# Optimization experiments

Measured on AMD Instinct MI355X. Metric: run time of the kernel, lower is better.

Reference implementation:

```python
import jax, jax.numpy as jnp
import numpy as np

N = 10000
IN_DIM = 512
OUT_DIM = 128
E = 262144


def setup_inputs() -> dict:
    key = jax.random.key(0)
    ks = jax.random.split(key, 7)
    x = jax.random.normal(ks[0], (N, IN_DIM), dtype=jnp.float32)
    adj = jax.random.uniform(ks[1], (N, N), dtype=jnp.float32) * (1.0 / N)
    # xavier-ish scaled params
    weight = jax.random.normal(ks[2], (IN_DIM, OUT_DIM), dtype=jnp.float32) * (1.0 / np.sqrt(IN_DIM))
    weight_two = jax.random.normal(ks[3], (2 * OUT_DIM, OUT_DIM), dtype=jnp.float32) * (1.0 / np.sqrt(2 * OUT_DIM))
    weight_three = jax.random.normal(ks[4], (2 * OUT_DIM, 1), dtype=jnp.float32) * (1.0 / np.sqrt(2 * OUT_DIM))
    train_edges = jax.random.randint(ks[5], (E, 2), 0, N, dtype=jnp.int32)
    train_false_edges = jax.random.randint(ks[6], (E, 2), 0, N, dtype=jnp.int32)
    return {
        "x": x,
        "adj": adj,
        "weight": weight,
        "weight_two": weight_two,
        "weight_three": weight_three,
        "train_edges": train_edges,
        "train_false_edges": train_false_edges,
    }


def reference(x, adj, weight, weight_two, weight_three, train_edges, train_false_edges):
    # encode: z = adj @ (x @ W)   -> [N, OUT_DIM]
    z = adj @ (x @ weight)
    # decode: vectorized per-edge gather of both endpoints
    edges = jnp.concatenate([train_edges, train_false_edges], axis=0)  # [2E, 2]
    zi = z[edges[:, 0]]  # [2E, OUT_DIM]
    zj = z[edges[:, 1]]  # [2E, OUT_DIM]
    z_pair = jnp.concatenate([zi, zj], axis=1)          # [2E, 2*OUT_DIM]
    z_mult = zi * zj                                     # [2E, OUT_DIM]
    z_pair = jax.nn.relu(z_pair) @ weight_two            # [2E, OUT_DIM]
    logits = jnp.concatenate([z_pair, z_mult], axis=1) @ weight_three  # [2E, 1]
    return jax.nn.sigmoid(logits)
```

## Files before the change

kernel.cpp:

```cpp
#include <hip/hip_runtime.h>

#define N_NODES 10000
#define IN_DIM  512
#define OUT_DIM 128
#define NE      262144
#define K_DIM   10000
#define HT_S    10048

#define BM 64
#define BN 128
#define BK 64
#define SPLITS 8
#define KSTEPS_TOTAL 157
#define STEPS_PER_SPLIT 20

typedef __attribute__((ext_vector_type(8))) __bf16 bf16x8;
typedef __attribute__((ext_vector_type(4))) float  f32x4;

__device__ inline ushort f2bf(float f) {
    uint u = __float_as_uint(f);
    return (ushort)((u + 0x7fffu + ((u >> 16) & 1u)) >> 16);
}
__device__ inline float bf2f(ushort s) {
    return __uint_as_float(((uint)s) << 16);
}

__device__ __forceinline__ void gl2lds16(const void* g, void* l) {
    __builtin_amdgcn_global_load_lds(
        (const __attribute__((address_space(1))) void*)g,
        (__attribute__((address_space(3))) void*)l, 16, 0, 0);
}

__global__ __launch_bounds__(256) void k_prep(const float* __restrict__ w,
                                              const float* __restrict__ w2,
                                              const float* __restrict__ w3,
                                              ushort* __restrict__ WT,
                                              float* __restrict__ v,
                                              ushort* __restrict__ hT) {
    const int t = threadIdx.x;
    for (int idx = blockIdx.x * 256 + t; idx < IN_DIM * OUT_DIM; idx += gridDim.x * 256) {
        int k = idx >> 7, n = idx & 127;
        WT[n * IN_DIM + k] = f2bf(w[idx]);
    }
    if (blockIdx.x == 0) {
        float s = 0.f;
        for (int j = 0; j < OUT_DIM; ++j) s += w2[t * OUT_DIM + j] * w3[j];
        v[t] = s;
    }
    if (blockIdx.x == 1) {
        for (int idx = t; idx < 128 * (HT_S - N_NODES); idx += 256) {
            int c = idx / (HT_S - N_NODES), r = idx % (HT_S - N_NODES);
            hT[(size_t)c * HT_S + N_NODES + r] = 0;
        }
    }
}

__global__ __launch_bounds__(128) void k_xw(const float* __restrict__ x,
                                            const ushort* __restrict__ WT,
                                            ushort* __restrict__ hT) {
    const int tid = threadIdx.x, wave = tid >> 6, lane = tid & 63;
    const int lr = lane & 15, lg = lane >> 4;
    const int arow = blockIdx.x * 32 + wave * 16 + lr;
    const bool aok = arow < N_NODES;
    const float* pA = x + (size_t)arow * IN_DIM;

    f32x4 acc[8];
#pragma unroll
    for (int nf = 0; nf < 8; ++nf) acc[nf] = (f32x4){0.f, 0.f, 0.f, 0.f};

#pragma unroll 2
    for (int st = 0; st < 8; ++st) {
        const int k0 = st * 64;
        bf16x8 abf[2];
#pragma unroll
        for (int kh = 0; kh < 2; ++kh) {
            float4 a0 = make_float4(0.f, 0.f, 0.f, 0.f), a1 = a0;
            if (aok) {
                a0 = *(const float4*)(pA + k0 + kh * 32 + lg * 8);
                a1 = *(const float4*)(pA + k0 + kh * 32 + lg * 8 + 4);
            }
            ushort* ap = (ushort*)&abf[kh];
            ap[0] = f2bf(a0.x); ap[1] = f2bf(a0.y); ap[2] = f2bf(a0.z); ap[3] = f2bf(a0.w);
            ap[4] = f2bf(a1.x); ap[5] = f2bf(a1.y); ap[6] = f2bf(a1.z); ap[7] = f2bf(a1.w);
        }
#pragma unroll
        for (int kh = 0; kh < 2; ++kh)
#pragma unroll
            for (int nf = 0; nf < 8; ++nf) {
                bf16x8 bfv = *(const bf16x8*)(WT + (size_t)(nf * 16 + lr) * IN_DIM + k0 + kh * 32 + lg * 8);
                acc[nf] = __builtin_amdgcn_mfma_f32_16x16x32_bf16(abf[kh], bfv, acc[nf], 0, 0, 0);
            }
    }

    const int m0 = blockIdx.x * 32 + wave * 16 + lg * 4;
    if (m0 < N_NODES) {
#pragma unroll
        for (int nf = 0; nf < 8; ++nf) {
            int c = nf * 16 + lr;
            ushort4 pk;
            pk.x = f2bf(acc[nf][0]); pk.y = f2bf(acc[nf][1]);
            pk.z = f2bf(acc[nf][2]); pk.w = f2bf(acc[nf][3]);
            *(ushort4*)(hT + (size_t)c * HT_S + m0) = pk;
        }
    }
}

__global__ __launch_bounds__(256) void k_adj(const float* __restrict__ adj,
                                             const ushort* __restrict__ hT,
                                             float* __restrict__ zp) {
    __shared__ float  As[BM * BK];
    __shared__ ushort Bs[BN * BK];

    const int tid = threadIdx.x, wave = tid >> 6, lane = tid & 63;
    const int lr = lane & 15, lg = lane >> 4;
    const int m0 = blockIdx.x * BM;
    const int split = blockIdx.y;
    const int step0 = split * STEPS_PER_SPLIT;
    const int step1 = min(step0 + STEPS_PER_SPLIT, KSTEPS_TOTAL);

    long  abase[4];
    char* aldst[4];
#pragma unroll
    for (int q = 0; q < 4; ++q) {
        int c = tid + q * 256;
        int row = c >> 4, ch = c & 15;
        int grow = m0 + row; if (grow > N_NODES - 1) grow = N_NODES - 1;
        abase[q] = (long)grow * K_DIM + (long)((ch ^ (row & 7)) * 4);
        aldst[q] = (char*)As + c * 16;
    }
    long  bbase[4];
    char* bldst[4];
#pragma unroll
    for (int q = 0; q < 4; ++q) {
        int c = tid + q * 256;
        int row = c >> 3, ch = c & 7;
        bbase[q] = (long)row * HT_S + (long)((ch ^ (row & 7)) * 8);
        bldst[q] = (char*)Bs + c * 16;
    }
    const long ALIMIT = (long)K_DIM * N_NODES - 4;

    f32x4 acc[8];
#pragma unroll
    for (int nf = 0; nf < 8; ++nf) acc[nf] = (f32x4){0.f, 0.f, 0.f, 0.f};

    const int  arow  = wave * 16 + lr;
    const int  asw   = (arow & 7) << 4;
    const int  abyte = arow * 256;
    const char* Ab = (const char*)As;
    const char* Bb = (const char*)Bs;

    for (int st = step0; st < step1; ++st) {
        const int k0 = st * BK;

#pragma unroll
        for (int q = 0; q < 4; ++q) {
            long off = abase[q] + k0;
            if (off > ALIMIT) off = ALIMIT;
            gl2lds16(adj + off, aldst[q]);
        }
#pragma unroll
        for (int q = 0; q < 4; ++q)
            gl2lds16(hT + (bbase[q] + k0), bldst[q]);

        __syncthreads();

#pragma unroll
        for (int kh = 0; kh < 2; ++kh) {
            int o0 = kh * 128 + lg * 32;
            float4 fa0 = *(const float4*)(Ab + abyte + ((o0)      ^ asw));
            float4 fa1 = *(const float4*)(Ab + abyte + ((o0 + 16) ^ asw));
            bf16x8 abf;
            ushort* ap = (ushort*)&abf;
            ap[0] = f2bf(fa0.x); ap[1] = f2bf(fa0.y); ap[2] = f2bf(fa0.z); ap[3] = f2bf(fa0.w);
            ap[4] = f2bf(fa1.x); ap[5] = f2bf(fa1.y); ap[6] = f2bf(fa1.z); ap[7] = f2bf(fa1.w);
#pragma unroll
            for (int nf = 0; nf < 8; ++nf) {
                int brow = nf * 16 + lr;
                bf16x8 bv = *(const bf16x8*)(Bb + brow * 128 + ((kh * 64 + lg * 16) ^ ((brow & 7) << 4)));
                acc[nf] = __builtin_amdgcn_mfma_f32_16x16x32_bf16(abf, bv, acc[nf], 0, 0, 0);
            }
        }

        __syncthreads();
    }

    float* out = zp + (size_t)split * N_NODES * OUT_DIM;
    const int orow = m0 + wave * 16 + lg * 4;
#pragma unroll
    for (int nf = 0; nf < 8; ++nf)
#pragma unroll
        for (int r = 0; r < 4; ++r) {
            int row = orow + r;
            if (row < N_NODES)
                out[(size_t)row * OUT_DIM + nf * 16 + lr] = acc[nf][r];
        }
}

__global__ __launch_bounds__(256) void k_node(const float* __restrict__ zp,
                                              const float* __restrict__ v,
                                              const float* __restrict__ w3,
                                              float* __restrict__ a,
                                              float* __restrict__ b,
                                              ushort* __restrict__ zb,
                                              ushort* __restrict__ zwb) {
    const int wave = threadIdx.x >> 6, lane = threadIdx.x & 63;
    const int i = blockIdx.x * 4 + wave;
    if (i >= N_NODES) return;
    const int k0 = lane, k1 = lane + 64;

    float z0 = 0.f, z1 = 0.f;
#pragma unroll
    for (int s = 0; s < SPLITS; ++s) {
        const float* row = zp + ((size_t)s * N_NODES + i) * OUT_DIM;
        z0 += row[k0];
        z1 += row[k1];
    }
    zb[(size_t)i * OUT_DIM + k0]  = f2bf(z0);
    zb[(size_t)i * OUT_DIM + k1]  = f2bf(z1);
    zwb[(size_t)i * OUT_DIM + k0] = f2bf(z0 * w3[OUT_DIM + k0]);
    zwb[(size_t)i * OUT_DIM + k1] = f2bf(z1 * w3[OUT_DIM + k1]);

    float ra = fmaxf(z0, 0.f) * v[k0] + fmaxf(z1, 0.f) * v[k1];
    float rb = fmaxf(z0, 0.f) * v[OUT_DIM + k0] + fmaxf(z1, 0.f) * v[OUT_DIM + k1];
#pragma unroll
    for (int off = 32; off; off >>= 1) {
        ra += __shfl_down(ra, off);
        rb += __shfl_down(rb, off);
    }
    if (lane == 0) { a[i] = ra; b[i] = rb; }
}

__global__ __launch_bounds__(256) void k_edge(const int* __restrict__ e_true,
                                              const int* __restrict__ e_false,
                                              const float* __restrict__ a,
                                              const float* __restrict__ b,
                                              const ushort* __restrict__ zb,
                                              const ushort* __restrict__ zwb,
                                              float* __restrict__ out) {
    const int lane = threadIdx.x & 63;
    const int half = lane >> 5, l32 = lane & 31;
    const int gw   = (blockIdx.x * blockDim.x + threadIdx.x) >> 6;
    const int nw   = (gridDim.x * blockDim.x) >> 6;

    for (int e = gw * 2 + half; e < 2 * NE; e += nw * 2) {
        int2 ij = (e < NE) ? ((const int2*)e_true)[e] : ((const int2*)e_false)[e - NE];
        int i = ij.x, j = ij.y;

        uint2 zwi = *(const uint2*)(zwb + (size_t)i * OUT_DIM + l32 * 4);
        uint2 zjv = *(const uint2*)(zb  + (size_t)j * OUT_DIM + l32 * 4);
        float d = bf2f((ushort)(zwi.x & 0xffffu)) * bf2f((ushort)(zjv.x & 0xffffu))
                + bf2f((ushort)(zwi.x >> 16))     * bf2f((ushort)(zjv.x >> 16))
                + bf2f((ushort)(zwi.y & 0xffffu)) * bf2f((ushort)(zjv.y & 0xffffu))
                + bf2f((ushort)(zwi.y >> 16))     * bf2f((ushort)(zjv.y >> 16));
#pragma unroll
        for (int off = 16; off; off >>= 1) d += __shfl_xor(d, off, 32);
        if (l32 == 0) {
            float logit = a[i] + b[j] + d;
            out[e] = 1.0f / (1.0f + __expf(-logit));
        }
    }
}

extern "C" void kernel_launch(void* const* d_in, const int* in_sizes, int n_in,
                              void* d_out, int out_size, void* d_ws, size_t ws_size,
                              hipStream_t stream) {
    const float* x      = (const float*)d_in[0];
    const float* adj    = (const float*)d_in[1];
    const float* w      = (const float*)d_in[2];
    const float* w2     = (const float*)d_in[3];
    const float* w3     = (const float*)d_in[4];
    const int* e_true   = (const int*)d_in[5];
    const int* e_false  = (const int*)d_in[6];
    float* out          = (float*)d_out;

    char* ws = (char*)d_ws;
    ushort* hT  = (ushort*)(ws);
    float*  zp  = (float*)(ws + 2572288);
    float*  v   = (float*)(ws + 43532288);
    float*  a   = (float*)(ws + 43533312);
    float*  b   = (float*)(ws + 43573312);
    ushort* zb  = (ushort*)(ws + 43613312);
    ushort* zwb = (ushort*)(ws + 46173312);
    ushort* WT  = (ushort*)(ws + 48733312);

    k_prep<<<64, 256, 0, stream>>>(w, w2, w3, WT, v, hT);
    k_xw<<<313, 128, 0, stream>>>(x, WT, hT);
    k_adj<<<dim3(157, SPLITS), 256, 0, stream>>>(adj, hT, zp);
    k_node<<<2500, 256, 0, stream>>>(zp, v, w3, a, b, zb, zwb);
    k_edge<<<2048, 256, 0, stream>>>(e_true, e_false, a, b, zb, zwb, out);
}
```

Before: 206.0 us.

## Double-buffer adj GEMM LDS tiles and store node embeddings as scaled fp8

The adj GEMM kernel now keeps two LDS buffers and issues the next tile's global-to-LDS loads before computing on the current one. It waits with a partial vmcnt, which is meant to hide memory latency behind the MFMA work. Separately, the per-node z and z*w3 tables are stored as software-encoded e4m3 fp8 with a 1024 scale, halving the bytes gathered per edge in the edge kernel. The fp8 step lowers precision of the dot-product term and adds decode ALU work. Doubling LDS use may also reduce occupancy.

Measured after the change: 223.9 us. 1.09x slower.

```diff
diff --git a/kernel.cpp b/kernel.cpp
--- a/kernel.cpp
+++ b/kernel.cpp
@@ -23,6 +23,28 @@
 }
 __device__ inline float bf2f(ushort s) {
     return __uint_as_float(((uint)s) << 16);
+}
+
+__device__ inline uint fp8e(float f) {
+    float a = fabsf(f);
+    uint s = (f < 0.f) ? 0x80u : 0u;
+    if (a < 0.0009765625f) return s;
+    if (a >= 448.f) return s | 0x7Eu;
+    if (a < 0.015625f) {
+        uint m = (uint)(a * 512.f + 0.5f);
+        return s | (m == 8u ? 0x08u : m);
+    }
+    int e; float fr = frexpf(a, &e);
+    uint m = (uint)((2.f * fr - 1.f) * 8.f + 0.5f);
+    uint E = (uint)(e + 6);
+    if (m == 8u) { m = 0u; E += 1u; }
+    return s | (E << 3) | m;
+}
+__device__ inline float fp8d(uint b) {
+    uint e = (b >> 3) & 15u, m = b & 7u;
+    float mag = (e == 0u) ? (float)m * 0.001953125f
+                          : __uint_as_float(((e + 120u) << 23) | (m << 20));
+    return (b & 0x80u) ? -mag : mag;
 }
 
 __device__ __forceinline__ void gl2lds16(const void* g, void* l) {
@@ -108,8 +130,8 @@
 __global__ __launch_bounds__(256) void k_adj(const float* __restrict__ adj,
                                              const ushort* __restrict__ hT,
                                              float* __restrict__ zp) {
-    __shared__ float  As[BM * BK];
-    __shared__ ushort Bs[BN * BK];
+    __shared__ float  As[2][BM * BK];
+    __shared__ ushort Bs[2][BN * BK];
 
     const int tid = threadIdx.x, wave = tid >> 6, lane = tid & 63;
     const int lr = lane & 15, lg = lane >> 4;
@@ -118,24 +140,22 @@
     const int step0 = split * STEPS_PER_SPLIT;
     const int step1 = min(step0 + STEPS_PER_SPLIT, KSTEPS_TOTAL);
 
-    long  abase[4];
-    char* aldst[4];
+    long abase[4]; uint aoff[4];
 #pragma unroll
     for (int q = 0; q < 4; ++q) {
         int c = tid + q * 256;
         int row = c >> 4, ch = c & 15;
         int grow = m0 + row; if (grow > N_NODES - 1) grow = N_NODES - 1;
         abase[q] = (long)grow * K_DIM + (long)((ch ^ (row & 7)) * 4);
-        aldst[q] = (char*)As + c * 16;
-    }
-    long  bbase[4];
-    char* bldst[4];
+        aoff[q]  = (uint)c * 16u;
+    }
+    long bbase[4]; uint boff[4];
 #pragma unroll
     for (int q = 0; q < 4; ++q) {
         int c = tid + q * 256;
         int row = c >> 3, ch = c & 7;
         bbase[q] = (long)row * HT_S + (long)((ch ^ (row & 7)) * 8);
-        bldst[q] = (char*)Bs + c * 16;
+        boff[q]  = (uint)c * 16u;
     }
     const long ALIMIT = (long)K_DIM * N_NODES - 4;
 
@@ -143,27 +163,39 @@
 #pragma unroll
     for (int nf = 0; nf < 8; ++nf) acc[nf] = (f32x4){0.f, 0.f, 0.f, 0.f};
 
-    const int  arow  = wave * 16 + lr;
-    const int  asw   = (arow & 7) << 4;
-    const int  abyte = arow * 256;
-    const char* Ab = (const char*)As;
-    const char* Bb = (const char*)Bs;
-
-    for (int st = step0; st < step1; ++st) {
+    const int arow  = wave * 16 + lr;
+    const int asw   = (arow & 7) << 4;
+    const int abyte = arow * 256;
+
+    auto stage = [&](int buf, int st) {
         const int k0 = st * BK;
-
+        char* Ad = (char*)&As[buf][0];
+        char* Bd = (char*)&Bs[buf][0];
 #pragma unroll
         for (int q = 0; q < 4; ++q) {
             long off = abase[q] + k0;
             if (off > ALIMIT) off = ALIMIT;
-            gl2lds16(adj + off, aldst[q]);
+            gl2lds16(adj + off, Ad + aoff[q]);
         }
 #pragma unroll
         for (int q = 0; q < 4; ++q)
-            gl2lds16(hT + (bbase[q] + k0), bldst[q]);
-
-        __syncthreads();
-
+            gl2lds16(hT + (bbase[q] + k0), Bd + boff[q]);
+    };
+
+    stage(0, step0);
+    int cur = 0;
+    for (int st = step0; st < step1; ++st) {
+        const bool hn = (st + 1 < step1);
+        if (hn) {
+            stage(cur ^ 1, st + 1);
+            asm volatile("s_waitcnt vmcnt(8)" ::: "memory");
+        } else {
+            asm volatile("s_waitcnt vmcnt(0)" ::: "memory");
+        }
+        __builtin_amdgcn_s_barrier();
+
+        const char* Ab = (const char*)&As[cur][0];
+        const char* Bb = (const char*)&Bs[cur][0];
 #pragma unroll
         for (int kh = 0; kh < 2; ++kh) {
             int o0 = kh * 128 + lg * 32;
@@ -180,8 +212,8 @@
                 acc[nf] = __builtin_amdgcn_mfma_f32_16x16x32_bf16(abf, bv, acc[nf], 0, 0, 0);
             }
         }
-
-        __syncthreads();
+        __builtin_amdgcn_s_barrier();
+        cur ^= 1;
     }
 
     float* out = zp + (size_t)split * N_NODES * OUT_DIM;
@@ -201,8 +233,8 @@
                                               const float* __restrict__ w3,
                                               float* __restrict__ a,
                                               float* __restrict__ b,
-                                              ushort* __restrict__ zb,
-                                              ushort* __restrict__ zwb) {
+                                              uchar* __restrict__ zb8,
+                                              uchar* __restrict__ zwb8) {
     const int wave = threadIdx.x >> 6, lane = threadIdx.x & 63;
     const int i = blockIdx.x * 4 + wave;
     if (i >= N_NODES) return;
@@ -215,10 +247,10 @@
         z0 += row[k0];
         z1 += row[k1];
     }
-    zb[(size_t)i * OUT_DIM + k0]  = f2bf(z0);
-    zb[(size_t)i * OUT_DIM + k1]  = f2bf(z1);
-    zwb[(size_t)i * OUT_DIM + k0] = f2bf(z0 * w3[OUT_DIM + k0]);
-    zwb[(size_t)i * OUT_DIM + k1] = f2bf(z1 * w3[OUT_DIM + k1]);
+    zb8 [(size_t)i * OUT_DIM + k0] = (uchar)fp8e(z0 * 1024.f);
+    zb8 [(size_t)i * OUT_DIM + k1] = (uchar)fp8e(z1 * 1024.f);
+    zwb8[(size_t)i * OUT_DIM + k0] = (uchar)fp8e(z0 * w3[OUT_DIM + k0] * 1024.f);
+    zwb8[(size_t)i * OUT_DIM + k1] = (uchar)fp8e(z1 * w3[OUT_DIM + k1] * 1024.f);
 
     float ra = fmaxf(z0, 0.f) * v[k0] + fmaxf(z1, 0.f) * v[k1];
     float rb = fmaxf(z0, 0.f) * v[OUT_DIM + k0] + fmaxf(z1, 0.f) * v[OUT_DIM + k1];
@@ -234,8 +266,8 @@
                                               const int* __restrict__ e_false,
                                               const float* __restrict__ a,
                                               const float* __restrict__ b,
-                                              const ushort* __restrict__ zb,
-                                              const ushort* __restrict__ zwb,
+                                              const uchar* __restrict__ zb8,
+                                              const uchar* __restrict__ zwb8,
                                               float* __restrict__ out) {
     const int lane = threadIdx.x & 63;
     const int half = lane >> 5, l32 = lane & 31;
@@ -246,16 +278,16 @@
         int2 ij = (e < NE) ? ((const int2*)e_true)[e] : ((const int2*)e_false)[e - NE];
         int i = ij.x, j = ij.y;
 
-        uint2 zwi = *(const uint2*)(zwb + (size_t)i * OUT_DIM + l32 * 4);
-        uint2 zjv = *(const uint2*)(zb  + (size_t)j * OUT_DIM + l32 * 4);
-        float d = bf2f((ushort)(zwi.x & 0xffffu)) * bf2f((ushort)(zjv.x & 0xffffu))
-                + bf2f((ushort)(zwi.x >> 16))     * bf2f((ushort)(zjv.x >> 16))
-                + bf2f((ushort)(zwi.y & 0xffffu)) * bf2f((ushort)(zjv.y & 0xffffu))
-                + bf2f((ushort)(zwi.y >> 16))     * bf2f((ushort)(zjv.y >> 16));
+        uint zw4 = *(const uint*)(zwb8 + (size_t)i * OUT_DIM + l32 * 4);
+        uint zj4 = *(const uint*)(zb8  + (size_t)j * OUT_DIM + l32 * 4);
+        float d = fp8d(zw4 & 0xffu)         * fp8d(zj4 & 0xffu)
+                + fp8d((zw4 >> 8)  & 0xffu) * fp8d((zj4 >> 8)  & 0xffu)
+                + fp8d((zw4 >> 16) & 0xffu) * fp8d((zj4 >> 16) & 0xffu)
+                + fp8d(zw4 >> 24)           * fp8d(zj4 >> 24);
 #pragma unroll
         for (int off = 16; off; off >>= 1) d += __shfl_xor(d, off, 32);
         if (l32 == 0) {
-            float logit = a[i] + b[j] + d;
+            float logit = a[i] + b[j] + d * 9.5367431640625e-7f;
             out[e] = 1.0f / (1.0f + __expf(-logit));
         }
     }
@@ -274,18 +306,18 @@
     float* out          = (float*)d_out;
 
     char* ws = (char*)d_ws;
-    ushort* hT  = (ushort*)(ws);
-    float*  zp  = (float*)(ws + 2572288);
-    float*  v   = (float*)(ws + 43532288);
-    float*  a   = (float*)(ws + 43533312);
-    float*  b   = (float*)(ws + 43573312);
-    ushort* zb  = (ushort*)(ws + 43613312);
-    ushort* zwb = (ushort*)(ws + 46173312);
-    ushort* WT  = (ushort*)(ws + 48733312);
+    ushort* hT   = (ushort*)(ws);
+    float*  zp   = (float*)(ws + 2572288);
+    float*  v    = (float*)(ws + 43532288);
+    float*  a    = (float*)(ws + 43533312);
+    float*  b    = (float*)(ws + 43573312);
+    uchar*  zb8  = (uchar*)(ws + 43613312);
+    uchar*  zwb8 = (uchar*)(ws + 44893312);
+    ushort* WT   = (ushort*)(ws + 46173312);
 
     k_prep<<<64, 256, 0, stream>>>(w, w2, w3, WT, v, hT);
     k_xw<<<313, 128, 0, stream>>>(x, WT, hT);
     k_adj<<<dim3(157, SPLITS), 256, 0, stream>>>(adj, hT, zp);
-    k_node<<<2500, 256, 0, stream>>>(zp, v, w3, a, b, zb, zwb);
-    k_edge<<<2048, 256, 0, stream>>>(e_true, e_false, a, b, zb, zwb, out);
-}
+    k_node<<<2500, 256, 0, stream>>>(zp, v, w3, a, b, zb8, zwb8);
+    k_edge<<<2048, 256, 0, stream>>>(e_true, e_false, a, b, zb8, zwb8, out);
+}
```

## Double the adj GEMM M tile with two MFMA row fragments per wave

Applied to the files above, without the earlier changes.

The adj @ hT kernel now uses 128-row tiles, with each wave computing two 16-row fragments that share each loaded B fragment. This halves the hT traffic and LDS B reads per unit of work. To keep the grid about the same size, split-K is doubled from 8 to 16, and the partial-sum buffer and workspace offsets grow to match. In exchange, k_node must reduce twice as many fp32 partials, which adds global memory traffic. LDS use per block also rises, which may lower occupancy.

Measured after the change: 209.8 us. About the same (+1.9%).

```diff
diff --git a/kernel.cpp b/kernel.cpp
--- a/kernel.cpp
+++ b/kernel.cpp
@@ -7,12 +7,12 @@
 #define K_DIM   10000
 #define HT_S    10048
 
-#define BM 64
+#define BM 128
 #define BN 128
 #define BK 64
-#define SPLITS 8
+#define SPLITS 16
 #define KSTEPS_TOTAL 157
-#define STEPS_PER_SPLIT 20
+#define STEPS_PER_SPLIT 10
 
 typedef __attribute__((ext_vector_type(8))) __bf16 bf16x8;
 typedef __attribute__((ext_vector_type(4))) float  f32x4;
@@ -118,10 +118,10 @@
     const int step0 = split * STEPS_PER_SPLIT;
     const int step1 = min(step0 + STEPS_PER_SPLIT, KSTEPS_TOTAL);
 
-    long  abase[4];
-    char* aldst[4];
-#pragma unroll
-    for (int q = 0; q < 4; ++q) {
+    long  abase[8];
+    char* aldst[8];
+#pragma unroll
+    for (int q = 0; q < 8; ++q) {
         int c = tid + q * 256;
         int row = c >> 4, ch = c & 15;
         int grow = m0 + row; if (grow > N_NODES - 1) grow = N_NODES - 1;
@@ -139,13 +139,14 @@
     }
     const long ALIMIT = (long)K_DIM * N_NODES - 4;
 
-    f32x4 acc[8];
-#pragma unroll
-    for (int nf = 0; nf < 8; ++nf) acc[nf] = (f32x4){0.f, 0.f, 0.f, 0.f};
-
-    const int  arow  = wave * 16 + lr;
-    const int  asw   = (arow & 7) << 4;
-    const int  abyte = arow * 256;
+    f32x4 acc[2][8];
+#pragma unroll
+    for (int mf = 0; mf < 2; ++mf)
+#pragma unroll
+        for (int nf = 0; nf < 8; ++nf) acc[mf][nf] = (f32x4){0.f, 0.f, 0.f, 0.f};
+
+    const int  arow0 = wave * 32 + lr;
+    const int  asw   = (arow0 & 7) << 4;
     const char* Ab = (const char*)As;
     const char* Bb = (const char*)Bs;
 
@@ -153,7 +154,7 @@
         const int k0 = st * BK;
 
 #pragma unroll
-        for (int q = 0; q < 4; ++q) {
+        for (int q = 0; q < 8; ++q) {
             long off = abase[q] + k0;
             if (off > ALIMIT) off = ALIMIT;
             gl2lds16(adj + off, aldst[q]);
@@ -166,18 +167,23 @@
 
 #pragma unroll
         for (int kh = 0; kh < 2; ++kh) {
-            int o0 = kh * 128 + lg * 32;
-            float4 fa0 = *(const float4*)(Ab + abyte + ((o0)      ^ asw));
-            float4 fa1 = *(const float4*)(Ab + abyte + ((o0 + 16) ^ asw));
-            bf16x8 abf;
-            ushort* ap = (ushort*)&abf;
-            ap[0] = f2bf(fa0.x); ap[1] = f2bf(fa0.y); ap[2] = f2bf(fa0.z); ap[3] = f2bf(fa0.w);
-            ap[4] = f2bf(fa1.x); ap[5] = f2bf(fa1.y); ap[6] = f2bf(fa1.z); ap[7] = f2bf(fa1.w);
+            const int o0 = kh * 128 + lg * 32;
+            bf16x8 abf[2];
+#pragma unroll
+            for (int mf = 0; mf < 2; ++mf) {
+                const int abyte = (arow0 + mf * 16) * 256;
+                float4 fa0 = *(const float4*)(Ab + abyte + ((o0)      ^ asw));
+                float4 fa1 = *(const float4*)(Ab + abyte + ((o0 + 16) ^ asw));
+                ushort* ap = (ushort*)&abf[mf];
+                ap[0] = f2bf(fa0.x); ap[1] = f2bf(fa0.y); ap[2] = f2bf(fa0.z); ap[3] = f2bf(fa0.w);
+                ap[4] = f2bf(fa1.x); ap[5] = f2bf(fa1.y); ap[6] = f2bf(fa1.z); ap[7] = f2bf(fa1.w);
+            }
 #pragma unroll
             for (int nf = 0; nf < 8; ++nf) {
                 int brow = nf * 16 + lr;
                 bf16x8 bv = *(const bf16x8*)(Bb + brow * 128 + ((kh * 64 + lg * 16) ^ ((brow & 7) << 4)));
-                acc[nf] = __builtin_amdgcn_mfma_f32_16x16x32_bf16(abf, bv, acc[nf], 0, 0, 0);
+                acc[0][nf] = __builtin_amdgcn_mfma_f32_16x16x32_bf16(abf[0], bv, acc[0][nf], 0, 0, 0);
+                acc[1][nf] = __builtin_amdgcn_mfma_f32_16x16x32_bf16(abf[1], bv, acc[1][nf], 0, 0, 0);
             }
         }
 
@@ -185,15 +191,18 @@
     }
 
     float* out = zp + (size_t)split * N_NODES * OUT_DIM;
-    const int orow = m0 + wave * 16 + lg * 4;
-#pragma unroll
-    for (int nf = 0; nf < 8; ++nf)
-#pragma unroll
-        for (int r = 0; r < 4; ++r) {
-            int row = orow + r;
-            if (row < N_NODES)
-                out[(size_t)row * OUT_DIM + nf * 16 + lr] = acc[nf][r];
-        }
+#pragma unroll
+    for (int mf = 0; mf < 2; ++mf) {
+        const int orow = m0 + wave * 32 + mf * 16 + lg * 4;
+#pragma unroll
+        for (int nf = 0; nf < 8; ++nf)
+#pragma unroll
+            for (int r = 0; r < 4; ++r) {
+                int row = orow + r;
+                if (row < N_NODES)
+                    out[(size_t)row * OUT_DIM + nf * 16 + lr] = acc[mf][nf][r];
+            }
+    }
 }
 
 __global__ __launch_bounds__(256) void k_node(const float* __restrict__ zp,
@@ -276,16 +285,16 @@
     char* ws = (char*)d_ws;
     ushort* hT  = (ushort*)(ws);
     float*  zp  = (float*)(ws + 2572288);
-    float*  v   = (float*)(ws + 43532288);
-    float*  a   = (float*)(ws + 43533312);
-    float*  b   = (float*)(ws + 43573312);
-    ushort* zb  = (ushort*)(ws + 43613312);
-    ushort* zwb = (ushort*)(ws + 46173312);
-    ushort* WT  = (ushort*)(ws + 48733312);
+    float*  v   = (float*)(ws + 84492288);
+    float*  a   = (float*)(ws + 84493312);
+    float*  b   = (float*)(ws + 84533312);
+    ushort* zb  = (ushort*)(ws + 84573312);
+    ushort* zwb = (ushort*)(ws + 87133312);
+    ushort* WT  = (ushort*)(ws + 89693312);
 
     k_prep<<<64, 256, 0, stream>>>(w, w2, w3, WT, v, hT);
     k_xw<<<313, 128, 0, stream>>>(x, WT, hT);
-    k_adj<<<dim3(157, SPLITS), 256, 0, stream>>>(adj, hT, zp);
+    k_adj<<<dim3(79, SPLITS), 256, 0, stream>>>(adj, hT, zp);
     k_node<<<2500, 256, 0, stream>>>(zp, v, w3, a, b, zb, zwb);
     k_edge<<<2048, 256, 0, stream>>>(e_true, e_false, a, b, zb, zwb, out);
 }
```

## Double adj GEMM row tile, load adj directly to registers, split xw by columns

Applied to the files above, without the earlier changes.

The adj GEMM tile grows from 64 to 128 rows. Each wave now computes two 16-row fragments, so every B (hT) fragment read from LDS feeds two MFMAs and hT traffic per output halves. The A operand (adj) is now loaded straight from global memory into registers instead of through LDS, which removes the A staging buffer and its LDS reads. k_xw is re-gridded into 16-row by 32-column single-wave blocks to expose more parallelism. The trade-offs are higher register pressure (two 8-fragment accumulator sets, capped with launch_bounds 256,3), uncoalesced per-row global loads of adj, and fewer blocks (79x8) in the dominant kernel.

New measurement: 208.8 us. About the same (+1.3%).

```diff
diff --git a/kernel.cpp b/kernel.cpp
--- a/kernel.cpp
+++ b/kernel.cpp
@@ -7,7 +7,7 @@
 #define K_DIM   10000
 #define HT_S    10048
 
-#define BM 64
+#define BM 128
 #define BN 128
 #define BK 64
 #define SPLITS 8
@@ -55,30 +55,27 @@
     }
 }
 
-__global__ __launch_bounds__(128) void k_xw(const float* __restrict__ x,
-                                            const ushort* __restrict__ WT,
-                                            ushort* __restrict__ hT) {
-    const int tid = threadIdx.x, wave = tid >> 6, lane = tid & 63;
+__global__ __launch_bounds__(64) void k_xw(const float* __restrict__ x,
+                                           const ushort* __restrict__ WT,
+                                           ushort* __restrict__ hT) {
+    const int lane = threadIdx.x;
     const int lr = lane & 15, lg = lane >> 4;
-    const int arow = blockIdx.x * 32 + wave * 16 + lr;
-    const bool aok = arow < N_NODES;
-    const float* pA = x + (size_t)arow * IN_DIM;
-
-    f32x4 acc[8];
-#pragma unroll
-    for (int nf = 0; nf < 8; ++nf) acc[nf] = (f32x4){0.f, 0.f, 0.f, 0.f};
-
-#pragma unroll 2
+    const int r0 = blockIdx.x * 16;
+    const int c0 = blockIdx.y * 32;
+    const float* pA = x + (size_t)(r0 + lr) * IN_DIM;
+
+    f32x4 acc[2];
+#pragma unroll
+    for (int nf = 0; nf < 2; ++nf) acc[nf] = (f32x4){0.f, 0.f, 0.f, 0.f};
+
+#pragma unroll
     for (int st = 0; st < 8; ++st) {
         const int k0 = st * 64;
         bf16x8 abf[2];
 #pragma unroll
         for (int kh = 0; kh < 2; ++kh) {
-            float4 a0 = make_float4(0.f, 0.f, 0.f, 0.f), a1 = a0;
-            if (aok) {
-                a0 = *(const float4*)(pA + k0 + kh * 32 + lg * 8);
-                a1 = *(const float4*)(pA + k0 + kh * 32 + lg * 8 + 4);
-            }
+            float4 a0 = *(const float4*)(pA + k0 + kh * 32 + lg * 8);
+            float4 a1 = *(const float4*)(pA + k0 + kh * 32 + lg * 8 + 4);
             ushort* ap = (ushort*)&abf[kh];
             ap[0] = f2bf(a0.x); ap[1] = f2bf(a0.y); ap[2] = f2bf(a0.z); ap[3] = f2bf(a0.w);
             ap[4] = f2bf(a1.x); ap[5] = f2bf(a1.y); ap[6] = f2bf(a1.z); ap[7] = f2bf(a1.w);
@@ -86,29 +83,26 @@
 #pragma unroll
         for (int kh = 0; kh < 2; ++kh)
 #pragma unroll
-            for (int nf = 0; nf < 8; ++nf) {
-                bf16x8 bfv = *(const bf16x8*)(WT + (size_t)(nf * 16 + lr) * IN_DIM + k0 + kh * 32 + lg * 8);
+            for (int nf = 0; nf < 2; ++nf) {
+                bf16x8 bfv = *(const bf16x8*)(WT + (size_t)(c0 + nf * 16 + lr) * IN_DIM + k0 + kh * 32 + lg * 8);
                 acc[nf] = __builtin_amdgcn_mfma_f32_16x16x32_bf16(abf[kh], bfv, acc[nf], 0, 0, 0);
             }
     }
 
-    const int m0 = blockIdx.x * 32 + wave * 16 + lg * 4;
-    if (m0 < N_NODES) {
-#pragma unroll
-        for (int nf = 0; nf < 8; ++nf) {
-            int c = nf * 16 + lr;
-            ushort4 pk;
-            pk.x = f2bf(acc[nf][0]); pk.y = f2bf(acc[nf][1]);
-            pk.z = f2bf(acc[nf][2]); pk.w = f2bf(acc[nf][3]);
-            *(ushort4*)(hT + (size_t)c * HT_S + m0) = pk;
-        }
-    }
-}
-
-__global__ __launch_bounds__(256) void k_adj(const float* __restrict__ adj,
-                                             const ushort* __restrict__ hT,
-                                             float* __restrict__ zp) {
-    __shared__ float  As[BM * BK];
+    const int m0 = r0 + lg * 4;
+#pragma unroll
+    for (int nf = 0; nf < 2; ++nf) {
+        int c = c0 + nf * 16 + lr;
+        ushort4 pk;
+        pk.x = f2bf(acc[nf][0]); pk.y = f2bf(acc[nf][1]);
+        pk.z = f2bf(acc[nf][2]); pk.w = f2bf(acc[nf][3]);
+        *(ushort4*)(hT + (size_t)c * HT_S + m0) = pk;
+    }
+}
+
+__global__ __launch_bounds__(256, 3) void k_adj(const float* __restrict__ adj,
+                                                const ushort* __restrict__ hT,
+                                                float* __restrict__ zp) {
     __shared__ ushort Bs[BN * BK];
 
     const int tid = threadIdx.x, wave = tid >> 6, lane = tid & 63;
@@ -118,16 +112,6 @@
     const int step0 = split * STEPS_PER_SPLIT;
     const int step1 = min(step0 + STEPS_PER_SPLIT, KSTEPS_TOTAL);
 
-    long  abase[4];
-    char* aldst[4];
-#pragma unroll
-    for (int q = 0; q < 4; ++q) {
-        int c = tid + q * 256;
-        int row = c >> 4, ch = c & 15;
-        int grow = m0 + row; if (grow > N_NODES - 1) grow = N_NODES - 1;
-        abase[q] = (long)grow * K_DIM + (long)((ch ^ (row & 7)) * 4);
-        aldst[q] = (char*)As + c * 16;
-    }
     long  bbase[4];
     char* bldst[4];
 #pragma unroll
@@ -137,63 +121,77 @@
         bbase[q] = (long)row * HT_S + (long)((ch ^ (row & 7)) * 8);
         bldst[q] = (char*)Bs + c * 16;
     }
-    const long ALIMIT = (long)K_DIM * N_NODES - 4;
-
-    f32x4 acc[8];
-#pragma unroll
-    for (int nf = 0; nf < 8; ++nf) acc[nf] = (f32x4){0.f, 0.f, 0.f, 0.f};
-
-    const int  arow  = wave * 16 + lr;
-    const int  asw   = (arow & 7) << 4;
-    const int  abyte = arow * 256;
-    const char* Ab = (const char*)As;
+
+    const int ar0 = min(m0 + wave * 32 + lr,      N_NODES - 1);
+    const int ar1 = min(m0 + wave * 32 + 16 + lr, N_NODES - 1);
+    const float* pA0 = adj + (size_t)ar0 * K_DIM;
+    const float* pA1 = adj + (size_t)ar1 * K_DIM;
+
+    f32x4 acc[2][8];
+#pragma unroll
+    for (int mf = 0; mf < 2; ++mf)
+#pragma unroll
+        for (int nf = 0; nf < 8; ++nf) acc[mf][nf] = (f32x4){0.f, 0.f, 0.f, 0.f};
+
     const char* Bb = (const char*)Bs;
 
     for (int st = step0; st < step1; ++st) {
         const int k0 = st * BK;
 
 #pragma unroll
-        for (int q = 0; q < 4; ++q) {
-            long off = abase[q] + k0;
-            if (off > ALIMIT) off = ALIMIT;
-            gl2lds16(adj + off, aldst[q]);
-        }
-#pragma unroll
         for (int q = 0; q < 4; ++q)
             gl2lds16(hT + (bbase[q] + k0), bldst[q]);
 
+        float4 fa[2][2][2];
+#pragma unroll
+        for (int kh = 0; kh < 2; ++kh) {
+            int kk = k0 + kh * 32 + lg * 8;
+            int kc = (kk <= K_DIM - 8) ? kk : (K_DIM - 8);
+            fa[0][kh][0] = *(const float4*)(pA0 + kc);
+            fa[0][kh][1] = *(const float4*)(pA0 + kc + 4);
+            fa[1][kh][0] = *(const float4*)(pA1 + kc);
+            fa[1][kh][1] = *(const float4*)(pA1 + kc + 4);
+        }
+
         __syncthreads();
 
-#pragma unroll
-        for (int kh = 0; kh < 2; ++kh) {
-            int o0 = kh * 128 + lg * 32;
-            float4 fa0 = *(const float4*)(Ab + abyte + ((o0)      ^ asw));
-            float4 fa1 = *(const float4*)(Ab + abyte + ((o0 + 16) ^ asw));
-            bf16x8 abf;
-            ushort* ap = (ushort*)&abf;
-            ap[0] = f2bf(fa0.x); ap[1] = f2bf(fa0.y); ap[2] = f2bf(fa0.z); ap[3] = f2bf(fa0.w);
-            ap[4] = f2bf(fa1.x); ap[5] = f2bf(fa1.y); ap[6] = f2bf(fa1.z); ap[7] = f2bf(fa1.w);
+        bf16x8 abf[2][2];
+#pragma unroll
+        for (int mf = 0; mf < 2; ++mf)
+#pragma unroll
+            for (int kh = 0; kh < 2; ++kh) {
+                ushort* ap = (ushort*)&abf[mf][kh];
+                const float* f0 = (const float*)&fa[mf][kh][0];
+#pragma unroll
+                for (int e = 0; e < 8; ++e) ap[e] = f2bf(f0[e]);
+            }
+
+#pragma unroll
+        for (int kh = 0; kh < 2; ++kh)
 #pragma unroll
             for (int nf = 0; nf < 8; ++nf) {
                 int brow = nf * 16 + lr;
                 bf16x8 bv = *(const bf16x8*)(Bb + brow * 128 + ((kh * 64 + lg * 16) ^ ((brow & 7) << 4)));
-                acc[nf] = __builtin_amdgcn_mfma_f32_16x16x32_bf16(abf, bv, acc[nf], 0, 0, 0);
-            }
-        }
+                acc[0][nf] = __builtin_amdgcn_mfma_f32_16x16x32_bf16(abf[0][kh], bv, acc[0][nf], 0, 0, 0);
+                acc[1][nf] = __builtin_amdgcn_mfma_f32_16x16x32_bf16(abf[1][kh], bv, acc[1][nf], 0, 0, 0);
+            }
 
         __syncthreads();
     }
 
     float* out = zp + (size_t)split * N_NODES * OUT_DIM;
-    const int orow = m0 + wave * 16 + lg * 4;
-#pragma unroll
-    for (int nf = 0; nf < 8; ++nf)
-#pragma unroll
-        for (int r = 0; r < 4; ++r) {
-            int row = orow + r;
-            if (row < N_NODES)
-                out[(size_t)row * OUT_DIM + nf * 16 + lr] = acc[nf][r];
-        }
+#pragma unroll
+    for (int mf = 0; mf < 2; ++mf) {
+        const int orow = m0 + wave * 32 + mf * 16 + lg * 4;
+#pragma unroll
+        for (int nf = 0; nf < 8; ++nf)
+#pragma unroll
+            for (int r = 0; r < 4; ++r) {
+                int row = orow + r;
+                if (row < N_NODES)
+                    out[(size_t)row * OUT_DIM + nf * 16 + lr] = acc[mf][nf][r];
+            }
+    }
 }
 
 __global__ __launch_bounds__(256) void k_node(const float* __restrict__ zp,
@@ -284,8 +282,8 @@
     ushort* WT  = (ushort*)(ws + 48733312);
 
     k_prep<<<64, 256, 0, stream>>>(w, w2, w3, WT, v, hT);
-    k_xw<<<313, 128, 0, stream>>>(x, WT, hT);
-    k_adj<<<dim3(157, SPLITS), 256, 0, stream>>>(adj, hT, zp);
+    k_xw<<<dim3(625, 4), 64, 0, stream>>>(x, WT, hT);
+    k_adj<<<dim3(79, SPLITS), 256, 0, stream>>>(adj, hT, zp);
     k_node<<<2500, 256, 0, stream>>>(zp, v, w3, a, b, zb, zwb);
     k_edge<<<2048, 256, 0, stream>>>(e_true, e_false, a, b, zb, zwb, out);
 }
```
